# Optimization experiments

Measured on AMD Instinct MI355X. Metric: run time of the kernel, lower is better.

Reference implementation:

```python
import jax, jax.numpy as jnp
import numpy as np

N_NODES = 50000
N_EDGES = 800000
H = 128   # hidden_dim
E = 64    # edge_dim
LN_EPS = 1e-5


def _layer_norm(x, g, b):
    m = jnp.mean(x, axis=-1, keepdims=True)
    v = jnp.mean(jnp.square(x - m), axis=-1, keepdims=True)
    return (x - m) * jax.lax.rsqrt(v + LN_EPS) * g + b


def _gelu(x):
    return jax.nn.gelu(x, approximate=False)  # torch default exact GELU


def setup_inputs() -> dict:
    key = jax.random.key(0)
    ks = jax.random.split(key, 24)

    def lin(k, fin, fout):
        kw, kb = jax.random.split(k)
        s = 1.0 / np.sqrt(fin)
        W = jax.random.uniform(kw, (fin, fout), jnp.float32, -s, s)
        b = jax.random.uniform(kb, (fout,), jnp.float32, -s, s)
        return W, b

    inp = {}
    inp["x"] = jax.random.normal(ks[0], (N_NODES, H), jnp.float32)
    inp["edge_emb"] = jax.random.normal(ks[1], (N_EDGES, E), jnp.float32)
    inp["time_weight"] = jax.random.uniform(ks[2], (N_EDGES, 1), jnp.float32)
    inp["message_node_scale"] = jax.random.uniform(ks[3], (N_NODES, 1), jnp.float32)
    inp["ln1_g"] = jnp.ones((H,), jnp.float32)
    inp["ln1_b"] = jnp.zeros((H,), jnp.float32)
    inp["ln2_g"] = jnp.ones((H,), jnp.float32)
    inp["ln2_b"] = jnp.zeros((H,), jnp.float32)
    inp["selfW"], inp["selfb"] = lin(ks[4], H, H)
    inp["msgW1"], inp["msgb1"] = lin(ks[5], H + E, H)
    inp["msgW2"], inp["msgb2"] = lin(ks[6], H, H)
    inp["gateW1"], inp["gateb1"] = lin(ks[7], 2 * H + E, H)
    inp["gateW2"], inp["gateb2"] = lin(ks[8], H, 1)
    inp["aggW"], inp["aggb"] = lin(ks[9], H, H)
    inp["ffnW1"], inp["ffnb1"] = lin(ks[10], H, 2 * H)
    inp["ffnW2"], inp["ffnb2"] = lin(ks[11], 2 * H, H)
    inp["edge_src"] = jax.random.randint(ks[12], (N_EDGES,), 0, N_NODES, jnp.int32)
    inp["edge_dst"] = jax.random.randint(ks[13], (N_EDGES,), 0, N_NODES, jnp.int32)
    return inp


def reference(x, edge_emb, time_weight, message_node_scale,
              ln1_g, ln1_b, ln2_g, ln2_b,
              selfW, selfb, msgW1, msgb1, msgW2, msgb2,
              gateW1, gateb1, gateW2, gateb2,
              aggW, aggb, ffnW1, ffnb1, ffnW2, ffnb2,
              edge_src, edge_dst):
    n_nodes = x.shape[0]
    n_edges = edge_dst.shape[0]

    h = _layer_norm(x, ln1_g, ln1_b)
    hs = h[edge_src]  # [NE, H]
    hd = h[edge_dst]  # [NE, H]

    msg = _gelu(jnp.concatenate([hs, edge_emb], -1) @ msgW1 + msgb1) @ msgW2 + msgb2
    gate = jax.nn.sigmoid(
        _gelu(jnp.concatenate([hd, hs, edge_emb], -1) @ gateW1 + gateb1) @ gateW2 + gateb2)
    edge_repr = gate * msg
    edge_repr = edge_repr * time_weight
    edge_scale = 0.5 * (message_node_scale[edge_src] + message_node_scale[edge_dst])
    edge_repr = edge_repr * edge_scale

    agg = jax.ops.segment_sum(edge_repr, edge_dst, num_segments=n_nodes)
    deg = jax.ops.segment_sum(jnp.ones((n_edges, 1), x.dtype), edge_dst,
                              num_segments=n_nodes)
    agg = agg / jnp.maximum(deg, 1.0)

    update = (h @ selfW + selfb) + (agg @ aggW + aggb)
    out = x + update  # residual; dropout is identity at inference

    h2 = _layer_norm(out, ln2_g, ln2_b)
    ffn_update = _gelu(h2 @ ffnW1 + ffnb1) @ ffnW2 + ffnb2
    out = out + ffn_update
    return (out, edge_repr)
```

## Files before the change

kernel.cpp:

```cpp
#include <hip/hip_runtime.h>


typedef __attribute__((ext_vector_type(8))) short short8;
typedef __attribute__((ext_vector_type(4))) float f32x4;

#define NN 50000
#define NEDGE 800000

#define MFMA(a, b, c) __builtin_amdgcn_mfma_f32_16x16x32_bf16(a, b, c, 0, 0, 0)

__device__ __forceinline__ unsigned short f2bf(float f) {
  unsigned int u = __float_as_uint(f);
  u += 0x7fffu + ((u >> 16) & 1u);
  return (unsigned short)(u >> 16);
}
__device__ __forceinline__ float bf2f(unsigned short u) {
  return __uint_as_float((unsigned int)u << 16);
}
__device__ __forceinline__ unsigned int cvtpk(float a, float b) {
  unsigned int d;
  asm("v_cvt_pk_bf16_f32 %0, %1, %2" : "=v"(d) : "v"(a), "v"(b));
  return d;
}
__device__ __forceinline__ float geluf(float x) {
  const float t = x * fmaf(-0.1029437f, x * x, -2.3022211f);
  return x * __builtin_amdgcn_rcpf(1.0f + exp2f(t));
}
__device__ __forceinline__ short8 ld8(const unsigned short* p) {
  return *reinterpret_cast<const short8*>(p);
}
__device__ __forceinline__ int swz256(int row, int byteoff) {
  return row * 256 + (byteoff ^ ((row & 15) << 4));
}
__device__ __forceinline__ int swz128(int row, int byteoff) {
  return row * 128 + (byteoff ^ ((row & 7) << 4));
}

__device__ __forceinline__ void ln_frags(const float* __restrict__ rowp,
                                         const float* __restrict__ g,
                                         const float* __restrict__ b, int koff,
                                         short8 a[4]) {
  f32x4 v[8];
#pragma unroll
  for (int s = 0; s < 4; s++) {
    v[2 * s] = *reinterpret_cast<const f32x4*>(rowp + s * 32 + koff);
    v[2 * s + 1] = *reinterpret_cast<const f32x4*>(rowp + s * 32 + koff + 4);
  }
  float sm = 0.f;
#pragma unroll
  for (int i = 0; i < 8; i++) sm += v[i][0] + v[i][1] + v[i][2] + v[i][3];
  sm += __shfl_xor(sm, 16);
  sm += __shfl_xor(sm, 32);
  const float mean = sm * 0.0078125f;
  float sq = 0.f;
#pragma unroll
  for (int i = 0; i < 8; i++) {
#pragma unroll
    for (int t = 0; t < 4; t++) {
      const float d = v[i][t] - mean;
      sq += d * d;
    }
  }
  sq += __shfl_xor(sq, 16);
  sq += __shfl_xor(sq, 32);
  const float rs = rsqrtf(sq * 0.0078125f + 1e-5f);
#pragma unroll
  for (int s = 0; s < 4; s++) {
    const f32x4 glo = *reinterpret_cast<const f32x4*>(g + s * 32 + koff);
    const f32x4 ghi = *reinterpret_cast<const f32x4*>(g + s * 32 + koff + 4);
    const f32x4 blo = *reinterpret_cast<const f32x4*>(b + s * 32 + koff);
    const f32x4 bhi = *reinterpret_cast<const f32x4*>(b + s * 32 + koff + 4);
    float y[8];
#pragma unroll
    for (int t = 0; t < 4; t++) {
      y[t] = (v[2 * s][t] - mean) * rs * glo[t] + blo[t];
      y[4 + t] = (v[2 * s + 1][t] - mean) * rs * ghi[t] + bhi[t];
    }
    union { unsigned int u[4]; short8 s8; } pk;
    pk.u[0] = cvtpk(y[0], y[1]);
    pk.u[1] = cvtpk(y[2], y[3]);
    pk.u[2] = cvtpk(y[4], y[5]);
    pk.u[3] = cvtpk(y[6], y[7]);
    a[s] = pk.s8;
  }
}

__global__ __launch_bounds__(256) void prep_kernel(
    const float* __restrict__ selfW, const float* __restrict__ msgW1,
    const float* __restrict__ msgW2, const float* __restrict__ gateW1,
    const float* __restrict__ aggW, const float* __restrict__ ffnW1,
    const float* __restrict__ ffnW2, unsigned short* __restrict__ wts) {
  const int idx = blockIdx.x * 256 + threadIdx.x;
  if (idx < 16384) {
    int n = idx >> 7, k = idx & 127;
    wts[idx] = f2bf(selfW[k * 128 + n]);
  } else if (idx < 32768) {
    int l = idx - 16384, n = l >> 7, k = l & 127;
    wts[idx] = f2bf(aggW[k * 128 + n]);
  } else if (idx < 57344) {
    int l = idx - 32768, n = l / 192, k = l - n * 192;
    wts[idx] = f2bf(msgW1[k * 128 + n]);
  } else if (idx < 73728) {
    int l = idx - 57344, n = l >> 7, k = l & 127;
    wts[idx] = f2bf(msgW2[k * 128 + n]);
  } else if (idx < 114688) {
    int l = idx - 73728, n = l / 320, k = l - n * 320;
    wts[idx] = f2bf(gateW1[k * 128 + n]);
  } else if (idx < 147456) {
    int l = idx - 114688, n = l >> 7, k = l & 127;
    wts[idx] = f2bf(ffnW1[k * 256 + n]);
  } else if (idx < 180224) {
    int l = idx - 147456, n = l >> 8, k = l & 255;
    wts[idx] = f2bf(ffnW2[k * 128 + n]);
  }
}

__global__ __launch_bounds__(256) void node_pre_kernel(
    const float* __restrict__ x, const float* __restrict__ ln1g,
    const float* __restrict__ ln1b, const unsigned short* __restrict__ wts,
    unsigned short* __restrict__ pd, unsigned short* __restrict__ psm) {
  const int wid = threadIdx.x >> 6, lane = threadIdx.x & 63;
  const int q = lane >> 4, r16 = lane & 15, koff = q * 8;
  const int r0 = blockIdx.x * 64 + wid * 16;
  const int row = min(r0 + r16, NN - 1);
  const unsigned short* gateW1T = wts + 73728;
  const unsigned short* msgW1T = wts + 32768;
  short8 a[4];
  ln_frags(x + (size_t)row * 128, ln1g, ln1b, koff, a);
  f32x4 acc[3][8];
#pragma unroll
  for (int t = 0; t < 3; t++)
#pragma unroll
    for (int nt = 0; nt < 8; nt++) acc[t][nt] = (f32x4){0.f, 0.f, 0.f, 0.f};
#pragma unroll
  for (int s = 0; s < 4; s++) {
    const int k0 = s * 32 + koff;
#pragma unroll
    for (int nt = 0; nt < 8; nt++) {
      const int c = nt * 16 + r16;
      acc[0][nt] = MFMA(a[s], ld8(gateW1T + c * 320 + k0), acc[0][nt]);
      acc[1][nt] = MFMA(a[s], ld8(gateW1T + c * 320 + 128 + k0), acc[1][nt]);
      acc[2][nt] = MFMA(a[s], ld8(msgW1T + c * 192 + k0), acc[2][nt]);
    }
  }
#pragma unroll
  for (int j = 0; j < 4; j++) {
    const int gr = r0 + q * 4 + j;
    if (gr < NN) {
#pragma unroll
      for (int nt = 0; nt < 8; nt++) {
        const int c = nt * 16 + r16;
        pd[(size_t)gr * 128 + c] = f2bf(acc[0][nt][j]);
        psm[(size_t)gr * 256 + c] = f2bf(acc[1][nt][j]);
        psm[(size_t)gr * 256 + 128 + c] = f2bf(acc[2][nt][j]);
      }
    }
  }
}

__global__ __launch_bounds__(256) void count_kernel(
    const int* __restrict__ edst, int* __restrict__ cnt) {
  const int e = blockIdx.x * 256 + threadIdx.x;
  atomicAdd(&cnt[edst[e]], 1);
}

__global__ __launch_bounds__(256) void scan_sums_kernel(
    const int* __restrict__ cnt, int* __restrict__ bsum) {
  const int gi = blockIdx.x * 256 + threadIdx.x;
  int v = (gi < NN) ? cnt[gi] : 0;
#pragma unroll
  for (int m = 1; m < 64; m <<= 1) v += __shfl_xor(v, m);
  __shared__ int wsum[4];
  if ((threadIdx.x & 63) == 0) wsum[threadIdx.x >> 6] = v;
  __syncthreads();
  if (threadIdx.x == 0)
    bsum[blockIdx.x] = wsum[0] + wsum[1] + wsum[2] + wsum[3];
}

__global__ __launch_bounds__(256) void scan_offsets_kernel(
    const int* __restrict__ bsum, int* __restrict__ boff, int nb) {
  __shared__ int tmp[256];
  const int tid = threadIdx.x;
  const int v = (tid < nb) ? bsum[tid] : 0;
  tmp[tid] = v;
  __syncthreads();
#pragma unroll
  for (int d = 1; d < 256; d <<= 1) {
    const int t = (tid >= d) ? tmp[tid - d] : 0;
    __syncthreads();
    tmp[tid] += t;
    __syncthreads();
  }
  if (tid < nb) boff[tid] = tmp[tid] - v;
}

__global__ __launch_bounds__(256) void scan_final_kernel(
    const int* __restrict__ cnt, const int* __restrict__ boff,
    int* __restrict__ row_start, int* __restrict__ cursor) {
  const int tid = threadIdx.x, lane = tid & 63, wid = tid >> 6;
  const int gi = blockIdx.x * 256 + tid;
  const int val = (gi < NN) ? cnt[gi] : 0;
  int v = val;
#pragma unroll
  for (int d = 1; d < 64; d <<= 1) {
    const int t = __shfl_up(v, d);
    if (lane >= d) v += t;
  }
  __shared__ int wsum[4];
  if (lane == 63) wsum[wid] = v;
  __syncthreads();
  int woff = 0;
  for (int w = 0; w < wid; ++w) woff += wsum[w];
  const int excl = (v - val) + woff + boff[blockIdx.x];
  if (gi < NN) {
    row_start[gi] = excl;
    cursor[gi] = excl;
  }
  if (gi == NN - 1) row_start[NN] = excl + val;
}

__global__ __launch_bounds__(256) void scatter_kernel(
    const int* __restrict__ esrc, const int* __restrict__ edst,
    const float* __restrict__ tw, const float* __restrict__ mns,
    int* __restrict__ cursor, int4* __restrict__ etab) {
  const int e = blockIdx.x * 256 + threadIdx.x;
  const int si = esrc[e];
  const int di = edst[e];
  const int pos = atomicAdd(&cursor[di], 1);
  const float sc = tw[e] * 0.5f * (mns[si] + mns[di]);
  int4 v;
  v.x = e;
  v.y = si;
  v.z = di;
  v.w = __float_as_int(sc);
  etab[pos] = v;
}

__global__ __launch_bounds__(512, 6) void edge_kernel(
    const float* __restrict__ emb, const int4* __restrict__ etab,
    const unsigned short* __restrict__ pd,
    const unsigned short* __restrict__ psm,
    const unsigned short* __restrict__ wts, const float* __restrict__ msgb1,
    const float* __restrict__ msgb2, const float* __restrict__ gateb1,
    const float* __restrict__ gateW2, const float* __restrict__ gateb2v,
    float* __restrict__ erout, float* __restrict__ aggf) {
  __shared__ __align__(16) char buf[64 * 256 + 64 * 256 + 64 * 128];
  __shared__ float p_s[4][64];
  __shared__ float G_s[64];
  __shared__ float sc_s[64];
  __shared__ int di_s[64], eidx_s[64];

  char* pgp = buf;
  char* pmp = buf + 16384;
  char* embp = buf + 32768;
  float* xbuf = (float*)buf;

  const int tid = threadIdx.x;
  const int lane = tid & 63;
  const int wid = tid >> 6;
  const int q = lane >> 4;
  const int r16 = lane & 15;
  const int koff = q * 8;
  const int mg = wid >> 2;
  const int ng = wid & 3;
  const int e0 = blockIdx.x * 64;

  const unsigned short* gateW1T = wts + 73728;
  const unsigned short* msgW1T = wts + 32768;
  const unsigned short* msgW2T = wts + 57344;

  if (tid < 64) {
    const int4 et = etab[e0 + tid];
    eidx_s[tid] = et.x;
    di_s[tid] = et.z;
    sc_s[tid] = __int_as_float(et.w);
  }

#pragma unroll
  for (int r = 0; r < 2; r++) {
    const int unit = tid + 512 * r;
    const int row = unit >> 4;
    const int c = unit & 15;
    const int4 et = etab[e0 + row];
    const int si = et.y, di = et.z;
    const short8 vd = ld8(pd + (size_t)di * 128 + c * 8);
    const short8 vs = ld8(psm + (size_t)si * 256 + c * 8);
    union { unsigned int u[4]; short8 s; } pk;
#pragma unroll
    for (int h = 0; h < 4; h++) {
      const float f0 =
          bf2f((unsigned short)vd[2 * h]) + bf2f((unsigned short)vs[2 * h]);
      const float f1 = bf2f((unsigned short)vd[2 * h + 1]) +
                       bf2f((unsigned short)vs[2 * h + 1]);
      pk.u[h] = cvtpk(f0, f1);
    }
    *reinterpret_cast<short8*>(pgp + swz256(row, c * 16)) = pk.s;
    *reinterpret_cast<short8*>(pmp + swz256(row, c * 16)) =
        ld8(psm + (size_t)si * 256 + 128 + c * 8);
  }
  if (tid < 256) {
    const int row = tid >> 2, c4 = tid & 3;
    const int e = etab[e0 + row].x;
#pragma unroll
    for (int i = 0; i < 4; i++) {
      const f32x4 v =
          *reinterpret_cast<const f32x4*>(emb + (size_t)e * 64 + c4 * 16 + i * 4);
      uint2 w;
      w.x = cvtpk(v[0], v[1]);
      w.y = cvtpk(v[2], v[3]);
      *reinterpret_cast<uint2*>(embp + swz128(row, c4 * 32 + i * 8)) = w;
    }
  }
  __syncthreads();

  int cc[2];
  float g1[2], w2[2], b1m[2], b2m[2];
#pragma unroll
  for (int i = 0; i < 2; i++) {
    cc[i] = ng * 32 + i * 16 + r16;
    g1[i] = gateb1[cc[i]];
    w2[i] = gateW2[cc[i]];
    b1m[i] = msgb1[cc[i]];
    b2m[i] = msgb2[cc[i]];
  }

  f32x4 accg[2][2], acc1[2][2];
#pragma unroll
  for (int m = 0; m < 2; m++)
#pragma unroll
    for (int i = 0; i < 2; i++) {
      accg[m][i] = (f32x4){0.f, 0.f, 0.f, 0.f};
      acc1[m][i] = (f32x4){0.f, 0.f, 0.f, 0.f};
    }
#pragma unroll
  for (int s = 0; s < 2; s++) {
    const int k0 = s * 32 + koff;
    short8 a[2];
#pragma unroll
    for (int m = 0; m < 2; m++)
      a[m] = *reinterpret_cast<const short8*>(
          embp + swz128(mg * 32 + m * 16 + r16, k0 * 2));
#pragma unroll
    for (int i = 0; i < 2; i++) {
      const short8 bg = ld8(gateW1T + cc[i] * 320 + 256 + k0);
      const short8 bm = ld8(msgW1T + cc[i] * 192 + 128 + k0);
#pragma unroll
      for (int m = 0; m < 2; m++) {
        accg[m][i] = MFMA(a[m], bg, accg[m][i]);
        acc1[m][i] = MFMA(a[m], bm, acc1[m][i]);
      }
    }
  }

#pragma unroll
  for (int m = 0; m < 2; m++) {
#pragma unroll
    for (int j = 0; j < 4; j++) {
      const int row = mg * 32 + m * 16 + q * 4 + j;
      float v = 0.f;
#pragma unroll
      for (int i = 0; i < 2; i++) {
        const float pg = bf2f(*reinterpret_cast<const unsigned short*>(
            pgp + swz256(row, cc[i] * 2)));
        v += geluf(accg[m][i][j] + pg + g1[i]) * w2[i];
      }
      v += __shfl_xor(v, 1);
      v += __shfl_xor(v, 2);
      v += __shfl_xor(v, 4);
      v += __shfl_xor(v, 8);
      if (r16 == 0) p_s[ng][row] = v;
    }
  }

#pragma unroll
  for (int m = 0; m < 2; m++) {
#pragma unroll
    for (int i = 0; i < 2; i++) {
#pragma unroll
      for (int j = 0; j < 4; j++) {
        const int row = mg * 32 + m * 16 + q * 4 + j;
        unsigned short* ap =
            reinterpret_cast<unsigned short*>(pmp + swz256(row, cc[i] * 2));
        const float pm = bf2f(*ap);
        *ap = f2bf(geluf(acc1[m][i][j] + pm + b1m[i]));
      }
    }
  }
  __syncthreads();

  if (tid < 64) {
    const float p = gateb2v[0] + p_s[0][tid] + p_s[1][tid] + p_s[2][tid] +
                    p_s[3][tid];
    G_s[tid] =
        sc_s[tid] * __builtin_amdgcn_rcpf(1.f + exp2f(-1.4426950f * p));
  }

  f32x4 acc2[2][2];
#pragma unroll
  for (int m = 0; m < 2; m++)
#pragma unroll
    for (int i = 0; i < 2; i++) acc2[m][i] = (f32x4){0.f, 0.f, 0.f, 0.f};
#pragma unroll
  for (int s = 0; s < 4; s++) {
    const int k0 = s * 32 + koff;
    short8 a[2];
#pragma unroll
    for (int m = 0; m < 2; m++)
      a[m] = *reinterpret_cast<const short8*>(
          pmp + swz256(mg * 32 + m * 16 + r16, k0 * 2));
#pragma unroll
    for (int i = 0; i < 2; i++) {
      const short8 b = ld8(msgW2T + cc[i] * 128 + k0);
#pragma unroll
      for (int m = 0; m < 2; m++) acc2[m][i] = MFMA(a[m], b, acc2[m][i]);
    }
  }
  __syncthreads();

#pragma unroll
  for (int m = 0; m < 2; m++)
#pragma unroll
    for (int i = 0; i < 2; i++)
#pragma unroll
      for (int j = 0; j < 4; j++) {
        const int row = mg * 32 + m * 16 + q * 4 + j;
        xbuf[row * 132 + cc[i]] = G_s[row] * (acc2[m][i][j] + b2m[i]);
      }
  __syncthreads();

#pragma unroll
  for (int u = 0; u < 4; u++) {
    const int unit = tid + u * 512;
    const int r = unit >> 5;
    const int f4 = unit & 31;
    const f32x4 val = *reinterpret_cast<const f32x4*>(&xbuf[r * 132 + f4 * 4]);
    *reinterpret_cast<f32x4*>(erout + (size_t)eidx_s[r] * 128 + f4 * 4) = val;
  }

  {
    const int col = tid & 127;
    const int qt = tid >> 7;
    const int rbeg = qt * 16, rend = rbeg + 16;
    float acc = 0.f;
    int prev = di_s[rbeg];
    for (int r = rbeg; r < rend; ++r) {
      const int d = di_s[r];
      if (d != prev) {
        atomicAdd(&aggf[(size_t)prev * 128 + col], acc);
        acc = 0.f;
        prev = d;
      }
      acc += xbuf[r * 132 + col];
    }
    atomicAdd(&aggf[(size_t)prev * 128 + col], acc);
  }
}

__global__ __launch_bounds__(256) void node1_kernel(
    const float* __restrict__ x, const float* __restrict__ ln1g,
    const float* __restrict__ ln1b, const float* __restrict__ aggf,
    const int* __restrict__ row_start, const unsigned short* __restrict__ wts,
    const float* __restrict__ selfb, const float* __restrict__ aggb,
    float* __restrict__ out1) {
  const int wid = threadIdx.x >> 6, lane = threadIdx.x & 63;
  const int q = lane >> 4, r16 = lane & 15, koff = q * 8;
  const int r0 = blockIdx.x * 64 + wid * 16;
  const int row = min(r0 + r16, NN - 1);
  const float inv = __builtin_amdgcn_rcpf(
      fmaxf((float)(row_start[row + 1] - row_start[row]), 1.0f));
  const unsigned short* selfWT = wts;
  const unsigned short* aggWT = wts + 16384;
  short8 a1[4];
  ln_frags(x + (size_t)row * 128, ln1g, ln1b, koff, a1);
  f32x4 acc[8];
#pragma unroll
  for (int nt = 0; nt < 8; nt++) acc[nt] = (f32x4){0.f, 0.f, 0.f, 0.f};
#pragma unroll
  for (int s = 0; s < 4; s++) {
    const int k0 = s * 32 + koff;
    const float* ap = aggf + (size_t)row * 128 + k0;
    const f32x4 f0 = *reinterpret_cast<const f32x4*>(ap);
    const f32x4 f1 = *reinterpret_cast<const f32x4*>(ap + 4);
    union { unsigned int u[4]; short8 s; } pk;
    pk.u[0] = cvtpk(f0[0] * inv, f0[1] * inv);
    pk.u[1] = cvtpk(f0[2] * inv, f0[3] * inv);
    pk.u[2] = cvtpk(f1[0] * inv, f1[1] * inv);
    pk.u[3] = cvtpk(f1[2] * inv, f1[3] * inv);
#pragma unroll
    for (int nt = 0; nt < 8; nt++) {
      acc[nt] = MFMA(a1[s], ld8(selfWT + (nt * 16 + r16) * 128 + k0), acc[nt]);
      acc[nt] = MFMA(pk.s, ld8(aggWT + (nt * 16 + r16) * 128 + k0), acc[nt]);
    }
  }
#pragma unroll
  for (int j = 0; j < 4; j++) {
    const int gr = r0 + q * 4 + j;
    if (gr < NN) {
#pragma unroll
      for (int nt = 0; nt < 8; nt++) {
        const int c = r16 + 16 * nt;
        out1[(size_t)gr * 128 + c] =
            x[(size_t)gr * 128 + c] + acc[nt][j] + selfb[c] + aggb[c];
      }
    }
  }
}

__global__ __launch_bounds__(256) void ffn_kernel(
    const float* __restrict__ out1, const float* __restrict__ ln2g,
    const float* __restrict__ ln2b, const unsigned short* __restrict__ wts,
    const float* __restrict__ b1, const float* __restrict__ b2,
    float* __restrict__ outp) {
  __shared__ unsigned short ts[4][16 * 264];
  const int wid = threadIdx.x >> 6, lane = threadIdx.x & 63;
  const int q = lane >> 4, r16 = lane & 15, koff = q * 8;
  const int r0 = blockIdx.x * 64 + wid * 16;
  const int row = min(r0 + r16, NN - 1);
  const unsigned short* W1T = wts + 114688;
  const unsigned short* W2T = wts + 147456;
  short8 a[4];
  ln_frags(out1 + (size_t)row * 128, ln2g, ln2b, koff, a);
  f32x4 acc1[16];
#pragma unroll
  for (int nt = 0; nt < 16; nt++) acc1[nt] = (f32x4){0.f, 0.f, 0.f, 0.f};
#pragma unroll
  for (int s = 0; s < 4; s++) {
    const int k0 = s * 32 + koff;
#pragma unroll
    for (int nt = 0; nt < 16; nt++)
      acc1[nt] = MFMA(a[s], ld8(W1T + (nt * 16 + r16) * 128 + k0), acc1[nt]);
  }
  unsigned short* tw_ = ts[wid];
#pragma unroll
  for (int nt = 0; nt < 16; nt++) {
    const int c = r16 + 16 * nt;
    const float bb = b1[c];
#pragma unroll
    for (int j = 0; j < 4; j++)
      tw_[(q * 4 + j) * 264 + c] = f2bf(geluf(acc1[nt][j] + bb));
  }
  __syncthreads();
  f32x4 acc2[8];
#pragma unroll
  for (int nt = 0; nt < 8; nt++) acc2[nt] = (f32x4){0.f, 0.f, 0.f, 0.f};
#pragma unroll
  for (int s = 0; s < 8; s++) {
    const int k0 = s * 32 + koff;
    const short8 av = *reinterpret_cast<const short8*>(tw_ + r16 * 264 + k0);
#pragma unroll
    for (int nt = 0; nt < 8; nt++)
      acc2[nt] = MFMA(av, ld8(W2T + (nt * 16 + r16) * 256 + k0), acc2[nt]);
  }
#pragma unroll
  for (int j = 0; j < 4; j++) {
    const int gr = r0 + q * 4 + j;
    if (gr < NN) {
#pragma unroll
      for (int nt = 0; nt < 8; nt++) {
        const int c = r16 + 16 * nt;
        outp[(size_t)gr * 128 + c] =
            out1[(size_t)gr * 128 + c] + acc2[nt][j] + b2[c];
      }
    }
  }
}

extern "C" void kernel_launch(void* const* d_in, const int* in_sizes, int n_in,
                              void* d_out, int out_size, void* d_ws,
                              size_t ws_size, hipStream_t stream) {
  (void)in_sizes; (void)n_in; (void)out_size; (void)ws_size;
  const float* x = (const float*)d_in[0];
  const float* emb = (const float*)d_in[1];
  const float* tw = (const float*)d_in[2];
  const float* mns = (const float*)d_in[3];
  const float* ln1g = (const float*)d_in[4];
  const float* ln1b = (const float*)d_in[5];
  const float* ln2g = (const float*)d_in[6];
  const float* ln2b = (const float*)d_in[7];
  const float* selfW = (const float*)d_in[8];
  const float* selfb = (const float*)d_in[9];
  const float* msgW1 = (const float*)d_in[10];
  const float* msgb1 = (const float*)d_in[11];
  const float* msgW2 = (const float*)d_in[12];
  const float* msgb2 = (const float*)d_in[13];
  const float* gateW1 = (const float*)d_in[14];
  const float* gateb1 = (const float*)d_in[15];
  const float* gateW2 = (const float*)d_in[16];
  const float* gateb2 = (const float*)d_in[17];
  const float* aggW = (const float*)d_in[18];
  const float* aggb = (const float*)d_in[19];
  const float* ffnW1 = (const float*)d_in[20];
  const float* ffnb1 = (const float*)d_in[21];
  const float* ffnW2 = (const float*)d_in[22];
  const float* ffnb2 = (const float*)d_in[23];
  const int* esrc = (const int*)d_in[24];
  const int* edst = (const int*)d_in[25];

  char* ws = (char*)d_ws;
  unsigned short* pdb = (unsigned short*)(ws);
  unsigned short* psmb = (unsigned short*)(ws + 25600000);
  float* out1 = (float*)(ws + 51200000);
  unsigned short* wts = (unsigned short*)(ws + 76800000);
  int* cnt = (int*)(ws + 77160448);
  int* row_start = (int*)(ws + 77360640);
  int* cursor = (int*)(ws + 77560832);
  int* bsum = (int*)(ws + 77761024);
  int* boff = (int*)(ws + 77762048);
  int4* etab = (int4*)(ws + 77763072);

  float* out_nodes = (float*)d_out;
  float* out_edges = out_nodes + (size_t)NN * 128;
  float* aggf = out_nodes;

  const int NB_SCAN = (NN + 255) / 256;

  prep_kernel<<<704, 256, 0, stream>>>(selfW, msgW1, msgW2, gateW1, aggW,
                                       ffnW1, ffnW2, wts);
  node_pre_kernel<<<782, 256, 0, stream>>>(x, ln1g, ln1b, wts, pdb, psmb);
  hipMemsetAsync(cnt, 0, 200192, stream);
  hipMemsetAsync(aggf, 0, (size_t)NN * 128 * 4, stream);
  count_kernel<<<3125, 256, 0, stream>>>(edst, cnt);
  scan_sums_kernel<<<NB_SCAN, 256, 0, stream>>>(cnt, bsum);
  scan_offsets_kernel<<<1, 256, 0, stream>>>(bsum, boff, NB_SCAN);
  scan_final_kernel<<<NB_SCAN, 256, 0, stream>>>(cnt, boff, row_start, cursor);
  scatter_kernel<<<3125, 256, 0, stream>>>(esrc, edst, tw, mns, cursor, etab);
  edge_kernel<<<12500, 512, 0, stream>>>(emb, etab, pdb, psmb, wts, msgb1,
                                         msgb2, gateb1, gateW2, gateb2,
                                         out_edges, aggf);
  node1_kernel<<<782, 256, 0, stream>>>(x, ln1g, ln1b, aggf, row_start, wts,
                                        selfb, aggb, out1);
  ffn_kernel<<<782, 256, 0, stream>>>(out1, ln2g, ln2b, wts, ffnb1, ffnb2,
                                      out_nodes);
}
```

Measured before the change: 658.7 us.

## Split edge kernel into gate and message warp groups; fold memsets into kernels

New measurement: 809.5 us. 1.23x slower.

```diff
diff --git a/kernel.cpp b/kernel.cpp
--- a/kernel.cpp
+++ b/kernel.cpp
@@ -21,6 +21,9 @@
   unsigned int d;
   asm("v_cvt_pk_bf16_f32 %0, %1, %2" : "=v"(d) : "v"(a), "v"(b));
   return d;
+}
+__device__ __forceinline__ unsigned short f2bf1(float a) {
+  return (unsigned short)cvtpk(a, a);
 }
 __device__ __forceinline__ float geluf(float x) {
   const float t = x * fmaf(-0.1029437f, x * x, -2.3022211f);
@@ -89,8 +92,10 @@
     const float* __restrict__ selfW, const float* __restrict__ msgW1,
     const float* __restrict__ msgW2, const float* __restrict__ gateW1,
     const float* __restrict__ aggW, const float* __restrict__ ffnW1,
-    const float* __restrict__ ffnW2, unsigned short* __restrict__ wts) {
+    const float* __restrict__ ffnW2, unsigned short* __restrict__ wts,
+    int* __restrict__ cnt) {
   const int idx = blockIdx.x * 256 + threadIdx.x;
+  if (idx <= NN) cnt[idx] = 0;
   if (idx < 16384) {
     int n = idx >> 7, k = idx & 127;
     wts[idx] = f2bf(selfW[k * 128 + n]);
@@ -118,11 +123,21 @@
 __global__ __launch_bounds__(256) void node_pre_kernel(
     const float* __restrict__ x, const float* __restrict__ ln1g,
     const float* __restrict__ ln1b, const unsigned short* __restrict__ wts,
-    unsigned short* __restrict__ pd, unsigned short* __restrict__ psm) {
+    unsigned short* __restrict__ pd, unsigned short* __restrict__ psm,
+    float* __restrict__ aggf) {
   const int wid = threadIdx.x >> 6, lane = threadIdx.x & 63;
   const int q = lane >> 4, r16 = lane & 15, koff = q * 8;
   const int r0 = blockIdx.x * 64 + wid * 16;
   const int row = min(r0 + r16, NN - 1);
+  {
+    const int t = blockIdx.x * 256 + threadIdx.x;
+    const f32x4 z = (f32x4){0.f, 0.f, 0.f, 0.f};
+#pragma unroll
+    for (int k = 0; k < 8; k++) {
+      const int pos = t + k * 200192;
+      if (pos < NN * 32) reinterpret_cast<f32x4*>(aggf)[pos] = z;
+    }
+  }
   const unsigned short* gateW1T = wts + 73728;
   const unsigned short* msgW1T = wts + 32768;
   short8 a[4];
@@ -236,7 +251,7 @@
   etab[pos] = v;
 }
 
-__global__ __launch_bounds__(512, 6) void edge_kernel(
+__global__ __launch_bounds__(512, 4) void edge_kernel(
     const float* __restrict__ emb, const int4* __restrict__ etab,
     const unsigned short* __restrict__ pd,
     const unsigned short* __restrict__ psm,
@@ -245,7 +260,6 @@
     const float* __restrict__ gateW2, const float* __restrict__ gateb2v,
     float* __restrict__ erout, float* __restrict__ aggf) {
   __shared__ __align__(16) char buf[64 * 256 + 64 * 256 + 64 * 128];
-  __shared__ float p_s[4][64];
   __shared__ float G_s[64];
   __shared__ float sc_s[64];
   __shared__ int di_s[64], eidx_s[64];
@@ -261,8 +275,6 @@
   const int q = lane >> 4;
   const int r16 = lane & 15;
   const int koff = q * 8;
-  const int mg = wid >> 2;
-  const int ng = wid & 3;
   const int e0 = blockIdx.x * 64;
 
   const unsigned short* gateW1T = wts + 73728;
@@ -298,134 +310,117 @@
     *reinterpret_cast<short8*>(pmp + swz256(row, c * 16)) =
         ld8(psm + (size_t)si * 256 + 128 + c * 8);
   }
-  if (tid < 256) {
-    const int row = tid >> 2, c4 = tid & 3;
+#pragma unroll
+  for (int r = 0; r < 2; r++) {
+    const int unit = tid + 512 * r;
+    const int row = unit >> 4;
+    const int c4 = unit & 15;
     const int e = etab[e0 + row].x;
-#pragma unroll
-    for (int i = 0; i < 4; i++) {
-      const f32x4 v =
-          *reinterpret_cast<const f32x4*>(emb + (size_t)e * 64 + c4 * 16 + i * 4);
-      uint2 w;
-      w.x = cvtpk(v[0], v[1]);
-      w.y = cvtpk(v[2], v[3]);
-      *reinterpret_cast<uint2*>(embp + swz128(row, c4 * 32 + i * 8)) = w;
-    }
+    const f32x4 v =
+        *reinterpret_cast<const f32x4*>(emb + (size_t)e * 64 + c4 * 4);
+    uint2 w;
+    w.x = cvtpk(v[0], v[1]);
+    w.y = cvtpk(v[2], v[3]);
+    *reinterpret_cast<uint2*>(embp + swz128(row, c4 * 8)) = w;
   }
   __syncthreads();
 
-  int cc[2];
-  float g1[2], w2[2], b1m[2], b2m[2];
-#pragma unroll
-  for (int i = 0; i < 2; i++) {
-    cc[i] = ng * 32 + i * 16 + r16;
-    g1[i] = gateb1[cc[i]];
-    w2[i] = gateW2[cc[i]];
-    b1m[i] = msgb1[cc[i]];
-    b2m[i] = msgb2[cc[i]];
-  }
-
-  f32x4 accg[2][2], acc1[2][2];
-#pragma unroll
-  for (int m = 0; m < 2; m++)
-#pragma unroll
-    for (int i = 0; i < 2; i++) {
-      accg[m][i] = (f32x4){0.f, 0.f, 0.f, 0.f};
-      acc1[m][i] = (f32x4){0.f, 0.f, 0.f, 0.f};
-    }
-#pragma unroll
-  for (int s = 0; s < 2; s++) {
-    const int k0 = s * 32 + koff;
-    short8 a[2];
-#pragma unroll
-    for (int m = 0; m < 2; m++)
-      a[m] = *reinterpret_cast<const short8*>(
-          embp + swz128(mg * 32 + m * 16 + r16, k0 * 2));
-#pragma unroll
-    for (int i = 0; i < 2; i++) {
-      const short8 bg = ld8(gateW1T + cc[i] * 320 + 256 + k0);
-      const short8 bm = ld8(msgW1T + cc[i] * 192 + 128 + k0);
-#pragma unroll
-      for (int m = 0; m < 2; m++) {
-        accg[m][i] = MFMA(a[m], bg, accg[m][i]);
-        acc1[m][i] = MFMA(a[m], bm, acc1[m][i]);
-      }
-    }
-  }
-
-#pragma unroll
-  for (int m = 0; m < 2; m++) {
+  const int R0 = (wid & 3) * 16;
+
+  if (wid < 4) {
+    f32x4 accg[8];
+#pragma unroll
+    for (int nt = 0; nt < 8; nt++) accg[nt] = (f32x4){0.f, 0.f, 0.f, 0.f};
+#pragma unroll
+    for (int s = 0; s < 2; s++) {
+      const int k0 = s * 32 + koff;
+      const short8 a = *reinterpret_cast<const short8*>(
+          embp + swz128(R0 + r16, k0 * 2));
+#pragma unroll
+      for (int nt = 0; nt < 8; nt++)
+        accg[nt] = MFMA(a, ld8(gateW1T + (nt * 16 + r16) * 320 + 256 + k0),
+                        accg[nt]);
+    }
+    float p[4] = {0.f, 0.f, 0.f, 0.f};
+#pragma unroll
+    for (int nt = 0; nt < 8; nt++) {
+      const int c = nt * 16 + r16;
+      const float b1 = gateb1[c];
+      const float w2v = gateW2[c];
+#pragma unroll
+      for (int j = 0; j < 4; j++) {
+        const float pg = bf2f(*reinterpret_cast<const unsigned short*>(
+            pgp + swz256(R0 + q * 4 + j, c * 2)));
+        p[j] += geluf(accg[nt][j] + pg + b1) * w2v;
+      }
+    }
 #pragma unroll
     for (int j = 0; j < 4; j++) {
-      const int row = mg * 32 + m * 16 + q * 4 + j;
-      float v = 0.f;
-#pragma unroll
-      for (int i = 0; i < 2; i++) {
-        const float pg = bf2f(*reinterpret_cast<const unsigned short*>(
-            pgp + swz256(row, cc[i] * 2)));
-        v += geluf(accg[m][i][j] + pg + g1[i]) * w2[i];
-      }
-      v += __shfl_xor(v, 1);
-      v += __shfl_xor(v, 2);
-      v += __shfl_xor(v, 4);
-      v += __shfl_xor(v, 8);
-      if (r16 == 0) p_s[ng][row] = v;
-    }
-  }
-
-#pragma unroll
-  for (int m = 0; m < 2; m++) {
-#pragma unroll
-    for (int i = 0; i < 2; i++) {
+      p[j] += __shfl_xor(p[j], 1);
+      p[j] += __shfl_xor(p[j], 2);
+      p[j] += __shfl_xor(p[j], 4);
+      p[j] += __shfl_xor(p[j], 8);
+    }
+    if (r16 == 0) {
+      const float gb2 = gateb2v[0];
 #pragma unroll
       for (int j = 0; j < 4; j++) {
-        const int row = mg * 32 + m * 16 + q * 4 + j;
-        unsigned short* ap =
-            reinterpret_cast<unsigned short*>(pmp + swz256(row, cc[i] * 2));
-        const float pm = bf2f(*ap);
-        *ap = f2bf(geluf(acc1[m][i][j] + pm + b1m[i]));
-      }
-    }
-  }
-  __syncthreads();
-
-  if (tid < 64) {
-    const float p = gateb2v[0] + p_s[0][tid] + p_s[1][tid] + p_s[2][tid] +
-                    p_s[3][tid];
-    G_s[tid] =
-        sc_s[tid] * __builtin_amdgcn_rcpf(1.f + exp2f(-1.4426950f * p));
-  }
-
-  f32x4 acc2[2][2];
-#pragma unroll
-  for (int m = 0; m < 2; m++)
-#pragma unroll
-    for (int i = 0; i < 2; i++) acc2[m][i] = (f32x4){0.f, 0.f, 0.f, 0.f};
-#pragma unroll
-  for (int s = 0; s < 4; s++) {
-    const int k0 = s * 32 + koff;
-    short8 a[2];
-#pragma unroll
-    for (int m = 0; m < 2; m++)
-      a[m] = *reinterpret_cast<const short8*>(
-          pmp + swz256(mg * 32 + m * 16 + r16, k0 * 2));
-#pragma unroll
-    for (int i = 0; i < 2; i++) {
-      const short8 b = ld8(msgW2T + cc[i] * 128 + k0);
-#pragma unroll
-      for (int m = 0; m < 2; m++) acc2[m][i] = MFMA(a[m], b, acc2[m][i]);
-    }
-  }
-  __syncthreads();
-
-#pragma unroll
-  for (int m = 0; m < 2; m++)
-#pragma unroll
-    for (int i = 0; i < 2; i++)
+        const int row = R0 + q * 4 + j;
+        G_s[row] = sc_s[row] *
+                   __builtin_amdgcn_rcpf(1.f + exp2f(-1.4426950f * (p[j] + gb2)));
+      }
+    }
+  } else {
+    f32x4 acc1[8];
+#pragma unroll
+    for (int nt = 0; nt < 8; nt++) acc1[nt] = (f32x4){0.f, 0.f, 0.f, 0.f};
+#pragma unroll
+    for (int s = 0; s < 2; s++) {
+      const int k0 = s * 32 + koff;
+      const short8 a = *reinterpret_cast<const short8*>(
+          embp + swz128(R0 + r16, k0 * 2));
+#pragma unroll
+      for (int nt = 0; nt < 8; nt++)
+        acc1[nt] =
+            MFMA(a, ld8(msgW1T + (nt * 16 + r16) * 192 + 128 + k0), acc1[nt]);
+    }
+#pragma unroll
+    for (int nt = 0; nt < 8; nt++) {
+      const int c = nt * 16 + r16;
+      const float b1m = msgb1[c];
 #pragma unroll
       for (int j = 0; j < 4; j++) {
-        const int row = mg * 32 + m * 16 + q * 4 + j;
-        xbuf[row * 132 + cc[i]] = G_s[row] * (acc2[m][i][j] + b2m[i]);
-      }
+        unsigned short* ap = reinterpret_cast<unsigned short*>(
+            pmp + swz256(R0 + q * 4 + j, c * 2));
+        *ap = f2bf1(geluf(acc1[nt][j] + bf2f(*ap) + b1m));
+      }
+    }
+    f32x4 acc2[8];
+#pragma unroll
+    for (int nt = 0; nt < 8; nt++) acc2[nt] = (f32x4){0.f, 0.f, 0.f, 0.f};
+#pragma unroll
+    for (int s = 0; s < 4; s++) {
+      const int k0 = s * 32 + koff;
+      const short8 a = *reinterpret_cast<const short8*>(
+          pmp + swz256(R0 + r16, k0 * 2));
+#pragma unroll
+      for (int nt = 0; nt < 8; nt++)
+        acc2[nt] =
+            MFMA(a, ld8(msgW2T + (nt * 16 + r16) * 128 + k0), acc2[nt]);
+    }
+    __syncthreads();
+#pragma unroll
+    for (int nt = 0; nt < 8; nt++) {
+      const int c = nt * 16 + r16;
+      const float b2 = msgb2[c];
+#pragma unroll
+      for (int j = 0; j < 4; j++) {
+        const int row = R0 + q * 4 + j;
+        xbuf[row * 132 + c] = G_s[row] * (acc2[nt][j] + b2);
+      }
+    }
+  }
+  if (wid < 4) __syncthreads();
   __syncthreads();
 
 #pragma unroll
@@ -537,7 +532,7 @@
     const float bb = b1[c];
 #pragma unroll
     for (int j = 0; j < 4; j++)
-      tw_[(q * 4 + j) * 264 + c] = f2bf(geluf(acc1[nt][j] + bb));
+      tw_[(q * 4 + j) * 264 + c] = f2bf1(geluf(acc1[nt][j] + bb));
   }
   __syncthreads();
   f32x4 acc2[8];
@@ -615,10 +610,9 @@
   const int NB_SCAN = (NN + 255) / 256;
 
   prep_kernel<<<704, 256, 0, stream>>>(selfW, msgW1, msgW2, gateW1, aggW,
-                                       ffnW1, ffnW2, wts);
-  node_pre_kernel<<<782, 256, 0, stream>>>(x, ln1g, ln1b, wts, pdb, psmb);
-  hipMemsetAsync(cnt, 0, 200192, stream);
-  hipMemsetAsync(aggf, 0, (size_t)NN * 128 * 4, stream);
+                                       ffnW1, ffnW2, wts, cnt);
+  node_pre_kernel<<<782, 256, 0, stream>>>(x, ln1g, ln1b, wts, pdb, psmb,
+                                           aggf);
   count_kernel<<<3125, 256, 0, stream>>>(edst, cnt);
   scan_sums_kernel<<<NB_SCAN, 256, 0, stream>>>(cnt, bsum);
   scan_offsets_kernel<<<1, 256, 0, stream>>>(bsum, boff, NB_SCAN);
```
